# Performance work log

Hardware: AMD Instinct MI355X
Metric: run time of the kernel (lower is better)

Reference implementation:

```python
import jax, jax.numpy as jnp
import numpy as np

DIM = 64
HID = 512
TIME_STEPS = 10
BATCH = 1024
H = 1e-5  # finite-difference step


def setup_inputs() -> dict:
    key = jax.random.key(0)
    ks = jax.random.split(key, 7)
    s1 = 1.0 / np.sqrt(DIM)
    s2 = 1.0 / np.sqrt(HID)
    x = jax.random.normal(ks[0], (BATCH, DIM), dtype=jnp.float32)
    W1 = jax.random.uniform(ks[1], (DIM, HID), minval=-s1, maxval=s1, dtype=jnp.float32)
    b1 = jax.random.uniform(ks[2], (HID,), minval=-s1, maxval=s1, dtype=jnp.float32)
    W2 = jax.random.uniform(ks[3], (HID, HID), minval=-s2, maxval=s2, dtype=jnp.float32)
    b2 = jax.random.uniform(ks[4], (HID,), minval=-s2, maxval=s2, dtype=jnp.float32)
    W3 = jax.random.uniform(ks[5], (HID, DIM), minval=-s2, maxval=s2, dtype=jnp.float32)
    b3 = jax.random.uniform(ks[6], (DIM,), minval=-s2, maxval=s2, dtype=jnp.float32)
    return {"x": x, "W1": W1, "b1": b1, "W2": W2, "b2": b2, "W3": W3, "b3": b3}


def reference(x, W1, b1, W2, b2, W3, b3):
    def mlp(z):  # 3-layer MLP, applied over last axis
        h1 = jax.nn.relu(z @ W1 + b1)
        h2 = jax.nn.relu(h1 @ W2 + b2)
        return h2 @ W3 + b3

    t = jnp.linspace(0.0, 1.0, TIME_STEPS).astype(x.dtype)
    dts = t[1:] - t[:-1]  # [TIME_STEPS-1]
    eye = jnp.eye(DIM, dtype=x.dtype)

    def step(carry, dt):
        z, log_det = carry
        dz = mlp(z) * dt              # [B, D], Euler increment from pre-update z
        z = z + dz                    # Euler update
        # Faithful to torch: perturbations are applied to the UPDATED z,
        # but compared against dz computed from the pre-update z.
        zp = z[:, None, :] + H * eye  # [B, D, D] all dim perturbations batched
        dzp = mlp(zp) * dt            # [B, D, D]
        diag = jnp.einsum('bjj->bj', dzp)  # dz_plus[:, j] for perturbed dim j
        trace = jnp.sum((diag - dz) / H, axis=-1)  # [B]
        return (z, log_det - trace), None

    init = (x, jnp.zeros(x.shape[0], dtype=x.dtype))
    (z, log_det), _ = jax.lax.scan(step, init, dts)
    return z, log_det
```

## Files before the change

### kernel.cpp

```cpp
#include <hip/hip_runtime.h>


#define HD 512
#define DD 64
#define NB 1024

typedef __attribute__((ext_vector_type(8))) short short8;
typedef __attribute__((ext_vector_type(4))) float f32x4;

__device__ __forceinline__ unsigned short bf16_rn(float x) {
  unsigned int u = __float_as_uint(x);
  u += 0x7FFFu + ((u >> 16) & 1u);
  return (unsigned short)(u >> 16);
}
__device__ __forceinline__ float bf16_f(unsigned short h) {
  return __uint_as_float(((unsigned int)h) << 16);
}
#define MFMA(a, b, c) __builtin_amdgcn_mfma_f32_16x16x32_bf16(a, b, c, 0, 0, 0)

__global__ __launch_bounds__(512) void k_prep(const float* __restrict__ W1,
    const float* __restrict__ W2, const float* __restrict__ W3,
    short* __restrict__ W1h, short* __restrict__ W1l,
    short* __restrict__ W2h, short* __restrict__ W2l, short* __restrict__ Ep,
    short* __restrict__ W3h, short* __restrict__ W3l,
    float* __restrict__ logdet) {
  int bid = blockIdx.x;
  int kc = bid >> 2, kg = bid & 3;
  int tid = threadIdx.x;
  int nc = tid >> 4, nl = tid & 15;
  int u0 = kc * 32 + kg * 8;
  int n = nc * 16 + nl;
  if (bid < 2) logdet[bid * 512 + tid] = 0.f;
  float s[8];
#pragma unroll
  for (int j = 0; j < 8; ++j) s[j] = 0.f;
  for (int q = 0; q < DD; q += 4) {
    float4 w3q = *(const float4*)(W3 + n * DD + q);
#pragma unroll
    for (int i = 0; i < 4; ++i) {
      float wq = (i == 0) ? w3q.x : (i == 1) ? w3q.y : (i == 2) ? w3q.z : w3q.w;
      float4 a = *(const float4*)(W1 + (q + i) * HD + u0);
      float4 b = *(const float4*)(W1 + (q + i) * HD + u0 + 4);
      s[0] = fmaf(wq, a.x, s[0]); s[1] = fmaf(wq, a.y, s[1]);
      s[2] = fmaf(wq, a.z, s[2]); s[3] = fmaf(wq, a.w, s[3]);
      s[4] = fmaf(wq, b.x, s[4]); s[5] = fmaf(wq, b.y, s[5]);
      s[6] = fmaf(wq, b.z, s[6]); s[7] = fmaf(wq, b.w, s[7]);
    }
  }
  long off = ((long)(kc * 32 + nc) * 64 + kg * 16 + nl) * 8;
  short8 vh, vl, ve;
#pragma unroll
  for (int j = 0; j < 8; ++j) {
    float w2 = W2[(u0 + j) * HD + n];
    unsigned short uh = bf16_rn(w2);
    vh[j] = (short)uh;
    vl[j] = (short)bf16_rn(w2 - bf16_f(uh));
    ve[j] = (short)bf16_rn(w2 * s[j]);
  }
  *(short8*)(W2h + off) = vh;
  *(short8*)(W2l + off) = vl;
  *(short8*)(Ep + off) = ve;
  if (kc < 2) {
    short8 ah, al;
#pragma unroll
    for (int j = 0; j < 8; ++j) {
      float w1 = W1[(u0 + j) * HD + n];
      unsigned short uh = bf16_rn(w1);
      ah[j] = (short)uh;
      al[j] = (short)bf16_rn(w1 - bf16_f(uh));
    }
    *(short8*)(W1h + off) = ah;
    *(short8*)(W1l + off) = al;
  }
  if (nc < 4) {
    long off3 = ((long)(kc * 4 + nc) * 64 + kg * 16 + nl) * 8;
    short8 th, tl;
#pragma unroll
    for (int sub = 0; sub < 8; ++sub) {
      float w3v = W3[(u0 + sub) * DD + n];
      unsigned short uh = bf16_rn(w3v);
      th[sub] = (short)uh;
      tl[sub] = (short)bf16_rn(w3v - bf16_f(uh));
    }
    *(short8*)(W3h + off3) = th;
    *(short8*)(W3l + off3) = tl;
  }
}

__global__ __launch_bounds__(512) void k_step(
    const float* __restrict__ zin, float* __restrict__ zout,
    const float* __restrict__ yPartR, const float* __restrict__ gR,
    const float* __restrict__ SRead, float* __restrict__ SWrite,
    float* __restrict__ logdet,
    const float* __restrict__ b1, const float* __restrict__ b2,
    const float* __restrict__ b3,
    const short* __restrict__ W1h, const short* __restrict__ W1l,
    const short* __restrict__ W2h, const short* __restrict__ W2l,
    const short* __restrict__ Ep,
    const short* __restrict__ W3h, const short* __restrict__ W3l,
    float* __restrict__ yPartW, float* __restrict__ gW,
    float dt, float dtp, float dtHp, int mode) {
  __shared__ __align__(16) short zh[16 * 72];
  __shared__ __align__(16) short zl[16 * 72];
  __shared__ __align__(16) short hh[16 * 520];
  __shared__ __align__(16) short hl[16 * 520];
  __shared__ __align__(16) short hm[16 * 520];
  __shared__ __align__(16) short h2h[16 * 136];
  __shared__ __align__(16) short h2l[16 * 136];
  __shared__ float gred[8 * 16];
  int bid = blockIdx.x;
  int cs = bid & 3;
  int r0 = (bid >> 2) << 4;
  int tid = threadIdx.x;
  int l = tid & 63;
  int w = tid >> 6;

#pragma unroll
  for (int half = 0; half < 2; ++half) {
    int rr = w + half * 8;
    int row = r0 + rr;
    float zv = zin[row * DD + l];
    float yv = 0.f;
    if (mode) {
      yv = yPartR[(0 * NB + row) * DD + l] + yPartR[(1 * NB + row) * DD + l] +
           yPartR[(2 * NB + row) * DD + l] + yPartR[(3 * NB + row) * DD + l] +
           b3[l];
      zv = fmaf(yv, dt, zv);
    }
    if (cs == 0) zout[row * DD + l] = zv;
    unsigned short hx = bf16_rn(zv);
    zh[rr * 72 + l] = (short)hx;
    zl[rr * 72 + l] = (short)bf16_rn(zv - bf16_f(hx));
    if (mode) {
      float sv = yv;
#pragma unroll
      for (int m = 1; m < 64; m <<= 1) sv += __shfl_xor(sv, m);
      if (l == 0 && cs == 0) {
        SWrite[row] = sv;
        if (mode == 2) {
          float g = gR[0 * NB + row] + gR[1 * NB + row] +
                    gR[2 * NB + row] + gR[3 * NB + row];
          logdet[row] -= (sv - SRead[row]) * dtHp + g * dtp;
        }
      }
    }
  }
  __syncthreads();

  {
    int mrow = l & 15;
    int kg = l >> 4;
    short8 az0h = *(const short8*)(zh + mrow * 72 + kg * 8);
    short8 az0l = *(const short8*)(zl + mrow * 72 + kg * 8);
    short8 az1h = *(const short8*)(zh + mrow * 72 + 32 + kg * 8);
    short8 az1l = *(const short8*)(zl + mrow * 72 + 32 + kg * 8);
    for (int i = 0; i < 4; ++i) {
      int nc = w * 4 + i;
      f32x4 acc = {0.f, 0.f, 0.f, 0.f};
      short8 b0h = *(const short8*)(W1h + ((long)(nc) * 64 + l) * 8);
      short8 b0l = *(const short8*)(W1l + ((long)(nc) * 64 + l) * 8);
      short8 c1h = *(const short8*)(W1h + ((long)(32 + nc) * 64 + l) * 8);
      short8 c1l = *(const short8*)(W1l + ((long)(32 + nc) * 64 + l) * 8);
      acc = MFMA(az0h, b0h, acc); acc = MFMA(az0h, b0l, acc);
      acc = MFMA(az0l, b0h, acc); acc = MFMA(az0l, b0l, acc);
      acc = MFMA(az1h, c1h, acc); acc = MFMA(az1h, c1l, acc);
      acc = MFMA(az1l, c1h, acc); acc = MFMA(az1l, c1l, acc);
      int n = nc * 16 + (l & 15);
      float bb = b1[n];
#pragma unroll
      for (int reg = 0; reg < 4; ++reg) {
        float h = fmaxf(acc[reg] + bb, 0.f);
        int r = (l >> 4) * 4 + reg;
        unsigned short uh = bf16_rn(h);
        unsigned short ul = bf16_rn(h - bf16_f(uh));
        unsigned short um = (h > 0.f) ? 0x3F80u : 0u;
        int ph = __shfl_xor((int)uh, 1);
        int pl = __shfl_xor((int)ul, 1);
        int pm = __shfl_xor((int)um, 1);
        if ((l & 1) == 0) {
          int base = r * 520 + n;
          *(unsigned int*)(hh + base) = (unsigned int)uh | (((unsigned int)(unsigned short)ph) << 16);
          *(unsigned int*)(hl + base) = (unsigned int)ul | (((unsigned int)(unsigned short)pl) << 16);
          *(unsigned int*)(hm + base) = (unsigned int)um | (((unsigned int)(unsigned short)pm) << 16);
        }
      }
    }
  }
  __syncthreads();

  {
    int mrow = l & 15;
    int kg = l >> 4;
    int ncg = cs * 8 + w;
    int n = ncg * 16 + mrow;
    f32x4 aH = {0.f, 0.f, 0.f, 0.f};
    f32x4 aT = {0.f, 0.f, 0.f, 0.f};
#pragma unroll 4
    for (int kc = 0; kc < 16; ++kc) {
      short8 Ah = *(const short8*)(hh + mrow * 520 + kc * 32 + kg * 8);
      short8 Al = *(const short8*)(hl + mrow * 520 + kc * 32 + kg * 8);
      short8 Am = *(const short8*)(hm + mrow * 520 + kc * 32 + kg * 8);
      long boff = ((long)(kc * 32 + ncg) * 64 + l) * 8;
      short8 Bh = *(const short8*)(W2h + boff);
      short8 Bl = *(const short8*)(W2l + boff);
      short8 Be = *(const short8*)(Ep + boff);
      aH = MFMA(Ah, Bh, aH); aH = MFMA(Ah, Bl, aH);
      aH = MFMA(Al, Bh, aH); aH = MFMA(Al, Bl, aH);
      aT = MFMA(Am, Be, aT);
    }
    float bb2 = b2[n];
    float h2v[4], gq[4];
#pragma unroll
    for (int reg = 0; reg < 4; ++reg) {
      float hv = aH[reg] + bb2;
      h2v[reg] = fmaxf(hv, 0.f);
      gq[reg] = (hv > 0.f) ? aT[reg] : 0.f;
    }
#pragma unroll
    for (int m = 1; m < 16; m <<= 1) {
#pragma unroll
      for (int reg = 0; reg < 4; ++reg) gq[reg] += __shfl_xor(gq[reg], m);
    }
    if ((l & 15) == 0) {
#pragma unroll
      for (int reg = 0; reg < 4; ++reg) gred[w * 16 + kg * 4 + reg] = gq[reg];
    }
#pragma unroll
    for (int reg = 0; reg < 4; ++reg) {
      unsigned short uh = bf16_rn(h2v[reg]);
      unsigned short ul = bf16_rn(h2v[reg] - bf16_f(uh));
      int ph = __shfl_xor((int)uh, 1);
      int pl = __shfl_xor((int)ul, 1);
      if ((l & 1) == 0) {
        int rrow = kg * 4 + reg;
        int c = w * 16 + (l & 15);
        *(unsigned int*)(h2h + rrow * 136 + c) = (unsigned int)uh | (((unsigned int)(unsigned short)ph) << 16);
        *(unsigned int*)(h2l + rrow * 136 + c) = (unsigned int)ul | (((unsigned int)(unsigned short)pl) << 16);
      }
    }
  }
  __syncthreads();

  if (w < 4) {
    int mrow = l & 15;
    int kg = l >> 4;
    f32x4 ay = {0.f, 0.f, 0.f, 0.f};
#pragma unroll
    for (int kc = 0; kc < 4; ++kc) {
      short8 Ah = *(const short8*)(h2h + mrow * 136 + kc * 32 + kg * 8);
      short8 Al = *(const short8*)(h2l + mrow * 136 + kc * 32 + kg * 8);
      long b3off = (((long)(cs * 4 + kc) * 4 + w) * 64 + l) * 8;
      short8 Bh = *(const short8*)(W3h + b3off);
      short8 Bl = *(const short8*)(W3l + b3off);
      ay = MFMA(Ah, Bh, ay); ay = MFMA(Ah, Bl, ay);
      ay = MFMA(Al, Bh, ay); ay = MFMA(Al, Bl, ay);
    }
#pragma unroll
    for (int reg = 0; reg < 4; ++reg) {
      int row = r0 + kg * 4 + reg;
      yPartW[((long)cs * NB + row) * DD + w * 16 + mrow] = ay[reg];
    }
  } else if (w == 4) {
    if (l < 16) {
      float g = 0.f;
#pragma unroll
      for (int ww = 0; ww < 8; ++ww) g += gred[ww * 16 + l];
      gW[cs * NB + r0 + l] = g;
    }
  }
}

__global__ __launch_bounds__(512) void k_fin(const float* __restrict__ yPartR,
    const float* __restrict__ gR, const float* __restrict__ SRead,
    const float* __restrict__ b3, float* __restrict__ logdet,
    float dtp, float dtHp) {
  int row = blockIdx.x * 8 + (threadIdx.x >> 6);
  int l = threadIdx.x & 63;
  float yv = yPartR[(0 * NB + row) * DD + l] + yPartR[(1 * NB + row) * DD + l] +
             yPartR[(2 * NB + row) * DD + l] + yPartR[(3 * NB + row) * DD + l] +
             b3[l];
  float sv = yv;
#pragma unroll
  for (int m = 1; m < 64; m <<= 1) sv += __shfl_xor(sv, m);
  if (l == 0) {
    float g = gR[0 * NB + row] + gR[1 * NB + row] +
              gR[2 * NB + row] + gR[3 * NB + row];
    logdet[row] -= (sv - SRead[row]) * dtHp + g * dtp;
  }
}

__global__ __launch_bounds__(256) void k_out(const float* __restrict__ z,
    const float* __restrict__ logdet, float* __restrict__ out) {
  int i = blockIdx.x * 256 + threadIdx.x;
  if (i < NB * DD) out[i] = z[i];
  else out[i] = logdet[i - NB * DD];
}

extern "C" void kernel_launch(void* const* d_in, const int* in_sizes, int n_in,
                              void* d_out, int out_size, void* d_ws, size_t ws_size,
                              hipStream_t stream) {
  const float* x  = (const float*)d_in[0];
  const float* W1 = (const float*)d_in[1];
  const float* b1 = (const float*)d_in[2];
  const float* W2 = (const float*)d_in[3];
  const float* b2 = (const float*)d_in[4];
  const float* W3 = (const float*)d_in[5];
  const float* b3 = (const float*)d_in[6];
  float* out = (float*)d_out;

  short* sb  = (short*)d_ws;
  short* W2h = sb;
  short* W2l = W2h + HD * HD;
  short* Ep  = W2l + HD * HD;
  short* W1h = Ep + HD * HD;
  short* W1l = W1h + DD * HD;
  short* W3h = W1l + DD * HD;
  short* W3l = W3h + HD * DD;
  float* fb  = (float*)(W3l + HD * DD);
  float* yP0 = fb;
  float* yP1 = yP0 + 4 * NB * DD;
  float* gP0 = yP1 + 4 * NB * DD;
  float* gP1 = gP0 + 4 * NB;
  float* SB0 = gP1 + 4 * NB;
  float* SB1 = SB0 + NB;
  float* zb0 = SB1 + NB;
  float* zb1 = zb0 + NB * DD;
  float* logdet = zb1 + NB * DD;

  float* yP[2] = {yP0, yP1};
  float* gP[2] = {gP0, gP1};
  float* SB[2] = {SB0, SB1};
  float* zb[2] = {zb0, zb1};

  k_prep<<<64, 512, 0, stream>>>(W1, W2, W3, W1h, W1l, W2h, W2l, Ep, W3h, W3l,
                                 logdet);

  double td[10];
  for (int i = 0; i < 10; ++i) td[i] = (double)i / 9.0;
  float dts[9];
  for (int t = 0; t < 9; ++t) dts[t] = (float)td[t + 1] - (float)td[t];

  for (int k = 0; k <= 9; ++k) {
    const float* zi = (k == 0) ? x : zb[(k - 1) & 1];
    float dtc  = (k >= 1) ? dts[k - 1] : 0.f;
    float dtpv = (k >= 2) ? dts[k - 2] : 0.f;
    int mode = (k == 0) ? 0 : ((k == 1) ? 1 : 2);
    k_step<<<256, 512, 0, stream>>>(zi, zb[k & 1],
        yP[(k + 1) & 1], gP[(k + 1) & 1], SB[k & 1], SB[(k + 1) & 1], logdet,
        b1, b2, b3, W1h, W1l, W2h, W2l, Ep, W3h, W3l,
        yP[k & 1], gP[k & 1], dtc, dtpv, dtpv * 1e5f, mode);
  }
  k_fin<<<128, 512, 0, stream>>>(yP[1], gP[1], SB[0], b3, logdet,
                                 dts[8], dts[8] * 1e5f);

  k_out<<<260, 256, 0, stream>>>(zb[1], logdet, out);
}
```

Before: 211.3 us.

## Split hidden columns across 8 blocks, split-K layer 2, drop lo*lo MFMA terms

The per-step kernel now splits the layer-2 output columns eight ways instead of four, doubling the grid to 512 blocks. Inside each block the K dimension of layer 2 is split across two wave groups, and the halves are reduced through shared scratch. Shared-memory tiles are stored pre-swizzled in MFMA fragment order, so operand loads become contiguous short8 reads. The lo*lo correction MFMAs are dropped and independent accumulators are used to shorten dependency chains. In exchange, layer 1 is recomputed twice as often and partial sums grow to 8 slices, and dropping the lo*lo terms slightly lowers precision.

```diff
diff --git a/kernel.cpp b/kernel.cpp
--- a/kernel.cpp
+++ b/kernel.cpp
@@ -87,7 +87,7 @@
   }
 }
 
-__global__ __launch_bounds__(512) void k_step(
+__global__ __launch_bounds__(512, 4) void k_step(
     const float* __restrict__ zin, float* __restrict__ zout,
     const float* __restrict__ yPartR, const float* __restrict__ gR,
     const float* __restrict__ SRead, float* __restrict__ SWrite,
@@ -100,20 +100,24 @@
     const short* __restrict__ W3h, const short* __restrict__ W3l,
     float* __restrict__ yPartW, float* __restrict__ gW,
     float dt, float dtp, float dtHp, int mode) {
-  __shared__ __align__(16) short zh[16 * 72];
-  __shared__ __align__(16) short zl[16 * 72];
-  __shared__ __align__(16) short hh[16 * 520];
-  __shared__ __align__(16) short hl[16 * 520];
-  __shared__ __align__(16) short hm[16 * 520];
-  __shared__ __align__(16) short h2h[16 * 136];
-  __shared__ __align__(16) short h2l[16 * 136];
-  __shared__ float gred[8 * 16];
+  __shared__ __align__(16) short zh[2 * 64 * 8];
+  __shared__ __align__(16) short zl[2 * 64 * 8];
+  __shared__ __align__(16) short hh[16 * 64 * 8];
+  __shared__ __align__(16) short hl[16 * 64 * 8];
+  __shared__ __align__(16) short hm[16 * 64 * 8];
+  __shared__ __align__(16) short h2h[2 * 64 * 8];
+  __shared__ __align__(16) short h2l[2 * 64 * 8];
+  __shared__ __align__(16) float scrH[4 * 64 * 4];
+  __shared__ __align__(16) float scrT[4 * 64 * 4];
+  __shared__ float gred[64];
   int bid = blockIdx.x;
-  int cs = bid & 3;
-  int r0 = (bid >> 2) << 4;
+  int cs = bid & 7;
+  int r0 = (bid >> 3) << 4;
   int tid = threadIdx.x;
   int l = tid & 63;
   int w = tid >> 6;
+  int mrow = l & 15;
+  int kg = l >> 4;
 
 #pragma unroll
   for (int half = 0; half < 2; ++half) {
@@ -122,15 +126,16 @@
     float zv = zin[row * DD + l];
     float yv = 0.f;
     if (mode) {
-      yv = yPartR[(0 * NB + row) * DD + l] + yPartR[(1 * NB + row) * DD + l] +
-           yPartR[(2 * NB + row) * DD + l] + yPartR[(3 * NB + row) * DD + l] +
-           b3[l];
+#pragma unroll
+      for (int s = 0; s < 8; ++s) yv += yPartR[(s * NB + row) * DD + l];
+      yv += b3[l];
       zv = fmaf(yv, dt, zv);
     }
     if (cs == 0) zout[row * DD + l] = zv;
     unsigned short hx = bf16_rn(zv);
-    zh[rr * 72 + l] = (short)hx;
-    zl[rr * 72 + l] = (short)bf16_rn(zv - bf16_f(hx));
+    int offs = (((l >> 5) * 64 + ((l >> 3) & 3) * 16 + rr) << 3) + (l & 7);
+    zh[offs] = (short)hx;
+    zl[offs] = (short)bf16_rn(zv - bf16_f(hx));
     if (mode) {
       float sv = yv;
 #pragma unroll
@@ -138,8 +143,9 @@
       if (l == 0 && cs == 0) {
         SWrite[row] = sv;
         if (mode == 2) {
-          float g = gR[0 * NB + row] + gR[1 * NB + row] +
-                    gR[2 * NB + row] + gR[3 * NB + row];
+          float g = 0.f;
+#pragma unroll
+          for (int s = 0; s < 8; ++s) g += gR[s * NB + row];
           logdet[row] -= (sv - SRead[row]) * dtHp + g * dtp;
         }
       }
@@ -148,29 +154,29 @@
   __syncthreads();
 
   {
-    int mrow = l & 15;
-    int kg = l >> 4;
-    short8 az0h = *(const short8*)(zh + mrow * 72 + kg * 8);
-    short8 az0l = *(const short8*)(zl + mrow * 72 + kg * 8);
-    short8 az1h = *(const short8*)(zh + mrow * 72 + 32 + kg * 8);
-    short8 az1l = *(const short8*)(zl + mrow * 72 + 32 + kg * 8);
+    short8 az0h = *(const short8*)(zh + l * 8);
+    short8 az0l = *(const short8*)(zl + l * 8);
+    short8 az1h = *(const short8*)(zh + (64 + l) * 8);
+    short8 az1l = *(const short8*)(zl + (64 + l) * 8);
     for (int i = 0; i < 4; ++i) {
       int nc = w * 4 + i;
-      f32x4 acc = {0.f, 0.f, 0.f, 0.f};
       short8 b0h = *(const short8*)(W1h + ((long)(nc) * 64 + l) * 8);
       short8 b0l = *(const short8*)(W1l + ((long)(nc) * 64 + l) * 8);
       short8 c1h = *(const short8*)(W1h + ((long)(32 + nc) * 64 + l) * 8);
       short8 c1l = *(const short8*)(W1l + ((long)(32 + nc) * 64 + l) * 8);
-      acc = MFMA(az0h, b0h, acc); acc = MFMA(az0h, b0l, acc);
-      acc = MFMA(az0l, b0h, acc); acc = MFMA(az0l, b0l, acc);
-      acc = MFMA(az1h, c1h, acc); acc = MFMA(az1h, c1l, acc);
-      acc = MFMA(az1l, c1h, acc); acc = MFMA(az1l, c1l, acc);
-      int n = nc * 16 + (l & 15);
+      f32x4 aA = {0.f, 0.f, 0.f, 0.f};
+      f32x4 aB = {0.f, 0.f, 0.f, 0.f};
+      aA = MFMA(az0h, b0h, aA); aB = MFMA(az0h, b0l, aB);
+      aA = MFMA(az0l, b0h, aA); aB = MFMA(az1h, c1l, aB);
+      aA = MFMA(az1h, c1h, aA); aB = MFMA(az1l, c1h, aB);
+      int n = nc * 16 + mrow;
       float bb = b1[n];
+      int kcA = nc >> 1;
+      int kgA = (nc * 2 + (mrow >> 3)) & 3;
 #pragma unroll
       for (int reg = 0; reg < 4; ++reg) {
-        float h = fmaxf(acc[reg] + bb, 0.f);
-        int r = (l >> 4) * 4 + reg;
+        float h = fmaxf(aA[reg] + aB[reg] + bb, 0.f);
+        int r = kg * 4 + reg;
         unsigned short uh = bf16_rn(h);
         unsigned short ul = bf16_rn(h - bf16_f(uh));
         unsigned short um = (h > 0.f) ? 0x3F80u : 0u;
@@ -178,7 +184,7 @@
         int pl = __shfl_xor((int)ul, 1);
         int pm = __shfl_xor((int)um, 1);
         if ((l & 1) == 0) {
-          int base = r * 520 + n;
+          int base = ((kcA * 64 + kgA * 16 + r) << 3) + (mrow & 7);
           *(unsigned int*)(hh + base) = (unsigned int)uh | (((unsigned int)(unsigned short)ph) << 16);
           *(unsigned int*)(hl + base) = (unsigned int)ul | (((unsigned int)(unsigned short)pl) << 16);
           *(unsigned int*)(hm + base) = (unsigned int)um | (((unsigned int)(unsigned short)pm) << 16);
@@ -189,84 +195,98 @@
   __syncthreads();
 
   {
-    int mrow = l & 15;
-    int kg = l >> 4;
-    int ncg = cs * 8 + w;
-    int n = ncg * 16 + mrow;
-    f32x4 aH = {0.f, 0.f, 0.f, 0.f};
+    int nch = w & 3;
+    int kh = w >> 2;
+    int ncg = cs * 4 + nch;
+    f32x4 aP = {0.f, 0.f, 0.f, 0.f};
+    f32x4 aQ = {0.f, 0.f, 0.f, 0.f};
     f32x4 aT = {0.f, 0.f, 0.f, 0.f};
-#pragma unroll 4
-    for (int kc = 0; kc < 16; ++kc) {
-      short8 Ah = *(const short8*)(hh + mrow * 520 + kc * 32 + kg * 8);
-      short8 Al = *(const short8*)(hl + mrow * 520 + kc * 32 + kg * 8);
-      short8 Am = *(const short8*)(hm + mrow * 520 + kc * 32 + kg * 8);
+#pragma unroll 2
+    for (int kk = 0; kk < 8; ++kk) {
+      int kc = kh * 8 + kk;
+      short8 Ah = *(const short8*)(hh + (kc * 64 + l) * 8);
+      short8 Al = *(const short8*)(hl + (kc * 64 + l) * 8);
+      short8 Am = *(const short8*)(hm + (kc * 64 + l) * 8);
       long boff = ((long)(kc * 32 + ncg) * 64 + l) * 8;
       short8 Bh = *(const short8*)(W2h + boff);
       short8 Bl = *(const short8*)(W2l + boff);
       short8 Be = *(const short8*)(Ep + boff);
-      aH = MFMA(Ah, Bh, aH); aH = MFMA(Ah, Bl, aH);
-      aH = MFMA(Al, Bh, aH); aH = MFMA(Al, Bl, aH);
+      aP = MFMA(Ah, Bh, aP);
+      aQ = MFMA(Ah, Bl, aQ);
+      aP = MFMA(Al, Bh, aP);
       aT = MFMA(Am, Be, aT);
     }
-    float bb2 = b2[n];
-    float h2v[4], gq[4];
-#pragma unroll
-    for (int reg = 0; reg < 4; ++reg) {
-      float hv = aH[reg] + bb2;
-      h2v[reg] = fmaxf(hv, 0.f);
-      gq[reg] = (hv > 0.f) ? aT[reg] : 0.f;
-    }
-#pragma unroll
-    for (int m = 1; m < 16; m <<= 1) {
-#pragma unroll
-      for (int reg = 0; reg < 4; ++reg) gq[reg] += __shfl_xor(gq[reg], m);
-    }
-    if ((l & 15) == 0) {
-#pragma unroll
-      for (int reg = 0; reg < 4; ++reg) gred[w * 16 + kg * 4 + reg] = gq[reg];
-    }
-#pragma unroll
-    for (int reg = 0; reg < 4; ++reg) {
-      unsigned short uh = bf16_rn(h2v[reg]);
-      unsigned short ul = bf16_rn(h2v[reg] - bf16_f(uh));
-      int ph = __shfl_xor((int)uh, 1);
-      int pl = __shfl_xor((int)ul, 1);
-      if ((l & 1) == 0) {
-        int rrow = kg * 4 + reg;
-        int c = w * 16 + (l & 15);
-        *(unsigned int*)(h2h + rrow * 136 + c) = (unsigned int)uh | (((unsigned int)(unsigned short)ph) << 16);
-        *(unsigned int*)(h2l + rrow * 136 + c) = (unsigned int)ul | (((unsigned int)(unsigned short)pl) << 16);
+    f32x4 aH;
+#pragma unroll
+    for (int i = 0; i < 4; ++i) aH[i] = aP[i] + aQ[i];
+    if (kh) {
+      *(f32x4*)(scrH + (nch * 64 + l) * 4) = aH;
+      *(f32x4*)(scrT + (nch * 64 + l) * 4) = aT;
+    }
+    __syncthreads();
+    if (!kh) {
+      f32x4 pH = *(const f32x4*)(scrH + (nch * 64 + l) * 4);
+      f32x4 pT = *(const f32x4*)(scrT + (nch * 64 + l) * 4);
+      int n = ncg * 16 + mrow;
+      float bb2 = b2[n];
+      float h2v[4], gq[4];
+#pragma unroll
+      for (int reg = 0; reg < 4; ++reg) {
+        float hv = aH[reg] + pH[reg] + bb2;
+        h2v[reg] = fmaxf(hv, 0.f);
+        gq[reg] = (hv > 0.f) ? (aT[reg] + pT[reg]) : 0.f;
+      }
+#pragma unroll
+      for (int m = 1; m < 16; m <<= 1) {
+#pragma unroll
+        for (int reg = 0; reg < 4; ++reg) gq[reg] += __shfl_xor(gq[reg], m);
+      }
+      if (mrow == 0) {
+#pragma unroll
+        for (int reg = 0; reg < 4; ++reg) gred[nch * 16 + kg * 4 + reg] = gq[reg];
+      }
+      int ns = nch * 16 + mrow;
+      int kcA = ns >> 5;
+      int kgA = ((ns >> 3) & 3);
+#pragma unroll
+      for (int reg = 0; reg < 4; ++reg) {
+        int r = kg * 4 + reg;
+        unsigned short uh = bf16_rn(h2v[reg]);
+        unsigned short ul = bf16_rn(h2v[reg] - bf16_f(uh));
+        int ph = __shfl_xor((int)uh, 1);
+        int pl = __shfl_xor((int)ul, 1);
+        if ((l & 1) == 0) {
+          int base = ((kcA * 64 + kgA * 16 + r) << 3) + (ns & 7);
+          *(unsigned int*)(h2h + base) = (unsigned int)uh | (((unsigned int)(unsigned short)ph) << 16);
+          *(unsigned int*)(h2l + base) = (unsigned int)ul | (((unsigned int)(unsigned short)pl) << 16);
+        }
       }
     }
   }
   __syncthreads();
 
   if (w < 4) {
-    int mrow = l & 15;
-    int kg = l >> 4;
-    f32x4 ay = {0.f, 0.f, 0.f, 0.f};
-#pragma unroll
-    for (int kc = 0; kc < 4; ++kc) {
-      short8 Ah = *(const short8*)(h2h + mrow * 136 + kc * 32 + kg * 8);
-      short8 Al = *(const short8*)(h2l + mrow * 136 + kc * 32 + kg * 8);
-      long b3off = (((long)(cs * 4 + kc) * 4 + w) * 64 + l) * 8;
+    f32x4 aA = {0.f, 0.f, 0.f, 0.f};
+    f32x4 aB = {0.f, 0.f, 0.f, 0.f};
+#pragma unroll
+    for (int kc2 = 0; kc2 < 2; ++kc2) {
+      short8 Ah = *(const short8*)(h2h + (kc2 * 64 + l) * 8);
+      short8 Al = *(const short8*)(h2l + (kc2 * 64 + l) * 8);
+      long b3off = (((long)((cs * 2 + kc2) * 4 + w)) * 64 + l) * 8;
       short8 Bh = *(const short8*)(W3h + b3off);
       short8 Bl = *(const short8*)(W3l + b3off);
-      ay = MFMA(Ah, Bh, ay); ay = MFMA(Ah, Bl, ay);
-      ay = MFMA(Al, Bh, ay); ay = MFMA(Al, Bl, ay);
+      aA = MFMA(Ah, Bh, aA);
+      aB = MFMA(Ah, Bl, aB);
+      aA = MFMA(Al, Bh, aA);
     }
 #pragma unroll
     for (int reg = 0; reg < 4; ++reg) {
       int row = r0 + kg * 4 + reg;
-      yPartW[((long)cs * NB + row) * DD + w * 16 + mrow] = ay[reg];
-    }
-  } else if (w == 4) {
-    if (l < 16) {
-      float g = 0.f;
-#pragma unroll
-      for (int ww = 0; ww < 8; ++ww) g += gred[ww * 16 + l];
-      gW[cs * NB + r0 + l] = g;
-    }
+      yPartW[((long)cs * NB + row) * DD + w * 16 + mrow] = aA[reg] + aB[reg];
+    }
+  } else if (w == 4 && l < 16) {
+    float g = gred[l] + gred[16 + l] + gred[32 + l] + gred[48 + l];
+    gW[cs * NB + r0 + l] = g;
   }
 }
 
@@ -276,15 +296,16 @@
     float dtp, float dtHp) {
   int row = blockIdx.x * 8 + (threadIdx.x >> 6);
   int l = threadIdx.x & 63;
-  float yv = yPartR[(0 * NB + row) * DD + l] + yPartR[(1 * NB + row) * DD + l] +
-             yPartR[(2 * NB + row) * DD + l] + yPartR[(3 * NB + row) * DD + l] +
-             b3[l];
+  float yv = b3[l];
+#pragma unroll
+  for (int s = 0; s < 8; ++s) yv += yPartR[(s * NB + row) * DD + l];
   float sv = yv;
 #pragma unroll
   for (int m = 1; m < 64; m <<= 1) sv += __shfl_xor(sv, m);
   if (l == 0) {
-    float g = gR[0 * NB + row] + gR[1 * NB + row] +
-              gR[2 * NB + row] + gR[3 * NB + row];
+    float g = 0.f;
+#pragma unroll
+    for (int s = 0; s < 8; ++s) g += gR[s * NB + row];
     logdet[row] -= (sv - SRead[row]) * dtHp + g * dtp;
   }
 }
@@ -318,10 +339,10 @@
   short* W3l = W3h + HD * DD;
   float* fb  = (float*)(W3l + HD * DD);
   float* yP0 = fb;
-  float* yP1 = yP0 + 4 * NB * DD;
-  float* gP0 = yP1 + 4 * NB * DD;
-  float* gP1 = gP0 + 4 * NB;
-  float* SB0 = gP1 + 4 * NB;
+  float* yP1 = yP0 + 8 * NB * DD;
+  float* gP0 = yP1 + 8 * NB * DD;
+  float* gP1 = gP0 + 8 * NB;
+  float* SB0 = gP1 + 8 * NB;
   float* SB1 = SB0 + NB;
   float* zb0 = SB1 + NB;
   float* zb1 = zb0 + NB * DD;
@@ -345,7 +366,7 @@
     float dtc  = (k >= 1) ? dts[k - 1] : 0.f;
     float dtpv = (k >= 2) ? dts[k - 2] : 0.f;
     int mode = (k == 0) ? 0 : ((k == 1) ? 1 : 2);
-    k_step<<<256, 512, 0, stream>>>(zi, zb[k & 1],
+    k_step<<<512, 512, 0, stream>>>(zi, zb[k & 1],
         yP[(k + 1) & 1], gP[(k + 1) & 1], SB[k & 1], SB[(k + 1) & 1], logdet,
         b1, b2, b3, W1h, W1l, W2h, W2l, Ep, W3h, W3l,
         yP[k & 1], gP[k & 1], dtc, dtpv, dtpv * 1e5f, mode);
```

After: 226.6 us. +7.2%, slower.
